# Kernel optimization log

Measured on AMD Instinct MI355X. Metric: run time of the kernel, lower is better.

Reference implementation:

```python
import jax, jax.numpy as jnp
import numpy as np

EPS_BN = 1e-3   # nn.BatchNorm1d(eps=0.001)
LAMDA = 1e-5    # Point_Attentation.lamda


def _bn(x, g, b, m, v):
    # inference-mode BatchNorm1d over last dim
    return (x - m) * (g * jax.lax.rsqrt(v + EPS_BN)) + b


def _forward(features_low, features_high,
             bott_W, bott_b, bott_gamma, bott_beta, bott_mean, bott_var,
             qkv_W, qkv_gamma, qkv_beta, qkv_mean, qkv_var,
             mlp_W, mlp_gamma, mlp_beta, mlp_mean, mlp_var,
             fus_W, fus_b, fus_gamma, fus_beta, fus_mean, fus_var,
             batch_size):
    N, C = features_low.shape
    B = batch_size
    n = N // B  # points per batch segment (equal-length segments)

    # ---- Point_Attentation: per-point channel mean, var over channels / (n-1) ----
    x = features_low
    mean = jnp.mean(x, axis=-1, keepdims=True)
    d = x - mean
    var = jnp.sum(d * d, axis=-1, keepdims=True) / (n - 1)
    e_t = d * d / (4.0 * (var + LAMDA)) + 0.5
    x = x + jax.nn.sigmoid(e_t) * x

    for i in range(3):
        y = jax.nn.relu(_bn(x @ bott_W[2 * i] + bott_b[2 * i],
                            bott_gamma[2 * i], bott_beta[2 * i], bott_mean[2 * i], bott_var[2 * i]))
        y = jax.nn.relu(_bn(y @ bott_W[2 * i + 1] + bott_b[2 * i + 1],
                            bott_gamma[2 * i + 1], bott_beta[2 * i + 1], bott_mean[2 * i + 1], bott_var[2 * i + 1]))
        x = x + y

    # ---- fusion: per-batch QKV attention between low (x) and high features ----
    low = x.reshape(B, n, C)
    high = features_high.reshape(B, n, C)

    q = _bn(jnp.einsum('bnc,cd->bnd', low, qkv_W[0]), qkv_gamma[0], qkv_beta[0], qkv_mean[0], qkv_var[0])
    k = _bn(jnp.einsum('bnc,cd->bnd', high, qkv_W[1]), qkv_gamma[1], qkv_beta[1], qkv_mean[1], qkv_var[1])
    v = _bn(jnp.einsum('bnc,cd->bnd', high, qkv_W[2]), qkv_gamma[2], qkv_beta[2], qkv_mean[2], qkv_var[2])

    scale = 1.0 / jnp.sqrt(jnp.asarray(256.0, dtype=q.dtype))  # normal_dim = 256
    attn = jax.nn.softmax(jnp.einsum('bqc,bkc->bqk', q, k) * scale, axis=-1)
    ao = jnp.einsum('bqk,bkc->bqc', attn, v)

    # mlp: (Linear no-bias -> BN -> Dropout(eval=id) -> ReLU) x2
    h = jax.nn.relu(_bn(jnp.einsum('bnc,cd->bnd', ao, mlp_W[0]), mlp_gamma[0], mlp_beta[0], mlp_mean[0], mlp_var[0]))
    h = jax.nn.relu(_bn(jnp.einsum('bnc,cd->bnd', h, mlp_W[1]), mlp_gamma[1], mlp_beta[1], mlp_mean[1], mlp_var[1]))

    # linear_fusion: Linear(2C->C, bias) -> BN -> ReLU
    cat = jnp.concatenate([low, h], axis=-1)  # [B, n, 2C]
    out = jax.nn.relu(_bn(jnp.einsum('bnc,cd->bnd', cat, fus_W) + fus_b, fus_gamma, fus_beta, fus_mean, fus_var))
    return out.reshape(N, C)


def setup_inputs() -> dict:
    key = jax.random.key(0)
    ks = jax.random.split(key, 16)
    N, C, B = 16384, 256, 4
    s = 0.05
    d = {}
    d['features_low'] = jax.random.normal(ks[0], (N, C), jnp.float32)
    d['features_high'] = jax.random.normal(ks[1], (N, C), jnp.float32)
    d['bott_W'] = jax.random.normal(ks[2], (6, C, C), jnp.float32) * s
    d['bott_b'] = jnp.zeros((6, C), jnp.float32)
    d['bott_gamma'] = jnp.ones((6, C), jnp.float32)
    d['bott_beta'] = jnp.zeros((6, C), jnp.float32)
    d['bott_mean'] = jnp.zeros((6, C), jnp.float32)
    d['bott_var'] = jnp.ones((6, C), jnp.float32)
    d['qkv_W'] = jax.random.normal(ks[3], (3, C, C), jnp.float32) * s
    d['qkv_gamma'] = jnp.ones((3, C), jnp.float32)
    d['qkv_beta'] = jnp.zeros((3, C), jnp.float32)
    d['qkv_mean'] = jnp.zeros((3, C), jnp.float32)
    d['qkv_var'] = jnp.ones((3, C), jnp.float32)
    d['mlp_W'] = jax.random.normal(ks[4], (2, C, C), jnp.float32) * s
    d['mlp_gamma'] = jnp.ones((2, C), jnp.float32)
    d['mlp_beta'] = jnp.zeros((2, C), jnp.float32)
    d['mlp_mean'] = jnp.zeros((2, C), jnp.float32)
    d['mlp_var'] = jnp.ones((2, C), jnp.float32)
    d['fus_W'] = jax.random.normal(ks[5], (2 * C, C), jnp.float32) * s
    d['fus_b'] = jnp.zeros((C,), jnp.float32)
    d['fus_gamma'] = jnp.ones((C,), jnp.float32)
    d['fus_beta'] = jnp.zeros((C,), jnp.float32)
    d['fus_mean'] = jnp.zeros((C,), jnp.float32)
    d['fus_var'] = jnp.ones((C,), jnp.float32)
    d['batch_size'] = B
    return d


def reference(features_low, features_high,
              bott_W, bott_b, bott_gamma, bott_beta, bott_mean, bott_var,
              qkv_W, qkv_gamma, qkv_beta, qkv_mean, qkv_var,
              mlp_W, mlp_gamma, mlp_beta, mlp_mean, mlp_var,
              fus_W, fus_b, fus_gamma, fus_beta, fus_mean, fus_var,
              batch_size):
    return _forward(features_low, features_high,
                    bott_W, bott_b, bott_gamma, bott_beta, bott_mean, bott_var,
                    qkv_W, qkv_gamma, qkv_beta, qkv_mean, qkv_var,
                    mlp_W, mlp_gamma, mlp_beta, mlp_mean, mlp_var,
                    fus_W, fus_b, fus_gamma, fus_beta, fus_mean, fus_var,
                    batch_size)
```

## Files before the change

### kernel.cpp

```cpp
#include <hip/hip_runtime.h>
#include <cstdint>
#include <cstddef>

typedef float v4f __attribute__((ext_vector_type(4)));
typedef float v2f __attribute__((ext_vector_type(2)));
typedef float v16f __attribute__((ext_vector_type(16)));
typedef short v8s __attribute__((ext_vector_type(8)));
typedef unsigned short v4u __attribute__((ext_vector_type(4)));

typedef unsigned short ubf;

#define NPTS 16384
#define CD   256
#define NBAT 4
#define NPB  4096

__device__ __forceinline__ float bf2f(ubf u) {
    union { unsigned u; float f; } c; c.u = ((unsigned)u) << 16; return c.f;
}
__device__ __forceinline__ ubf f2bf(float f) {
    union { float f; unsigned u; } c; c.f = f;
    unsigned u = c.u;
    u += 0x7fffu + ((u >> 16) & 1u);
    return (ubf)(u >> 16);
}

__global__ __launch_bounds__(256) void k_pre(
    const float* __restrict__ low, float* __restrict__ xout,
    const float* __restrict__ bott, const float* __restrict__ qkv,
    const float* __restrict__ mlp, const float* __restrict__ fus,
    ubf* __restrict__ wt) {
    const int bid = blockIdx.x;
    if (bid < 4096) {
        const int lane = threadIdx.x & 63;
        const int row  = bid * 4 + (threadIdx.x >> 6);
        const float* p = low + (size_t)row * CD + lane * 4;
        v4f v = *reinterpret_cast<const v4f*>(p);
        float d[4];
        float s = v[0] + v[1] + v[2] + v[3];
#pragma unroll
        for (int o = 32; o >= 1; o >>= 1) s += __shfl_xor(s, o);
        const float mean = s * (1.0f / 256.0f);
        float ss = 0.f;
#pragma unroll
        for (int i = 0; i < 4; ++i) { d[i] = v[i] - mean; ss += d[i] * d[i]; }
#pragma unroll
        for (int o = 32; o >= 1; o >>= 1) ss += __shfl_xor(ss, o);
        const float var = ss * (1.0f / 4095.0f);
        const float dn  = 1.0f / (4.0f * (var + 1e-5f));
        v4f o;
#pragma unroll
        for (int i = 0; i < 4; ++i) {
            const float e   = d[i] * d[i] * dn + 0.5f;
            const float sig = 1.0f / (1.0f + __expf(-e));
            o[i] = v[i] * (1.0f + sig);
        }
        *reinterpret_cast<v4f*>(xout + (size_t)row * CD + lane * 4) = o;
        return;
    }
    const int bid2 = bid - 4096;
    const int z = bid2 >> 7, r = bid2 & 127;
    const float* src; int K; size_t doff;
    if (z < 6)       { src = bott + (size_t)z * 65536;       K = 256; doff = (size_t)z * 65536; }
    else if (z < 9)  { src = qkv  + (size_t)(z - 6) * 65536; K = 256; doff = (size_t)z * 65536; }
    else if (z < 11) { src = mlp  + (size_t)(z - 9) * 65536; K = 256; doff = (size_t)z * 65536; }
    else             { src = fus;                            K = 512; doff = (size_t)11 * 65536; }
    const int kt = (r >> 3) * 32, nt = (r & 7) * 32;
    if (kt >= K) return;
    __shared__ ubf tile[32][33];
    const int tx = threadIdx.x & 31, ty = threadIdx.x >> 5;
#pragma unroll
    for (int i = 0; i < 4; ++i)
        tile[ty * 4 + i][tx] = f2bf(src[(size_t)(kt + ty * 4 + i) * 256 + nt + tx]);
    __syncthreads();
    ubf* dst = wt + doff;
#pragma unroll
    for (int i = 0; i < 4; ++i)
        dst[(size_t)(nt + ty * 4 + i) * K + kt + tx] = tile[tx][ty * 4 + i];
}

__global__ __launch_bounds__(256) void k_conv1(
    float* __restrict__ xA, const ubf* __restrict__ wT,
    const float* __restrict__ bb, const float* __restrict__ bg,
    const float* __restrict__ bbe, const float* __restrict__ bm_,
    const float* __restrict__ bv) {
    __shared__ __attribute__((aligned(16))) float xls[64 * 256];
    __shared__ __attribute__((aligned(16))) ubf   yls[64 * 256];

    const int lane = threadIdx.x & 63;
    const int w    = threadIdx.x >> 6;
    const int wr = w >> 1, wc = w & 1;
    const int q15 = lane & 15, g = lane >> 4;
    const int bm = blockIdx.x * 64;

    {
        float* xsrcb = xA + (size_t)bm * 256;
#pragma unroll
        for (int it = 0; it < 16; ++it) {
            const int L4 = (it * 256 + w * 64) * 4;
            const int Ll = L4 + lane * 4;
            const int row = Ll >> 8, col = (Ll & 255) ^ ((row & 7) << 3);
            __builtin_amdgcn_global_load_lds(
                (const __attribute__((address_space(1))) unsigned*)(xsrcb + row * 256 + col),
                (__attribute__((address_space(3))) unsigned*)(xls + L4), 16, 0, 0);
        }
    }
    __syncthreads();

    const int r0l = wr * 32 + q15;
#pragma unroll 1
    for (int s = 0; s < 3; ++s) {
        const ubf* W0 = wT + (size_t)(2 * s) * 65536;
        const ubf* W1 = wT + (size_t)(2 * s + 1) * 65536;

        v4f acc[2][8];
#pragma unroll
        for (int i = 0; i < 2; ++i)
#pragma unroll
            for (int j = 0; j < 8; ++j)
#pragma unroll
                for (int r = 0; r < 4; ++r) acc[i][j][r] = 0.f;
        for (int ks = 0; ks < 8; ++ks) {
            const int k0 = ks * 32 + g * 8;
            v8s afr[2], bfr[8];
#pragma unroll
            for (int mi = 0; mi < 2; ++mi) {
                const int row = r0l + mi * 16;
                const float* ap = &xls[row * 256 + (k0 ^ ((row & 7) << 3))];
                v4f a = *reinterpret_cast<const v4f*>(ap);
                v4f b = *reinterpret_cast<const v4f*>(ap + 4);
                v8s t;
#pragma unroll
                for (int j = 0; j < 4; ++j) { t[j] = (short)f2bf(a[j]); t[j + 4] = (short)f2bf(b[j]); }
                afr[mi] = t;
            }
#pragma unroll
            for (int ni = 0; ni < 8; ++ni)
                bfr[ni] = *reinterpret_cast<const v8s*>(W0 + (size_t)(wc * 128 + ni * 16 + q15) * 256 + k0);
#pragma unroll
            for (int mi = 0; mi < 2; ++mi)
#pragma unroll
                for (int ni = 0; ni < 8; ++ni)
                    acc[mi][ni] = __builtin_amdgcn_mfma_f32_16x16x32_bf16(afr[mi], bfr[ni], acc[mi][ni], 0, 0, 0);
        }
#pragma unroll
        for (int ni = 0; ni < 8; ++ni) {
            const int col = wc * 128 + ni * 16 + q15;
            const float sc  = bg[2 * s * 256 + col] * rsqrtf(bv[2 * s * 256 + col] + 1e-3f);
            const float tc  = bbe[2 * s * 256 + col] - bm_[2 * s * 256 + col] * sc;
            const float bia = bb[2 * s * 256 + col];
#pragma unroll
            for (int mi = 0; mi < 2; ++mi)
#pragma unroll
                for (int r = 0; r < 4; ++r) {
                    const int row = wr * 32 + mi * 16 + g * 4 + r;
                    float z = fmaxf((acc[mi][ni][r] + bia) * sc + tc, 0.f);
                    yls[row * 256 + (col ^ ((row & 7) << 3))] = f2bf(z);
                }
        }
        __syncthreads();

#pragma unroll
        for (int i = 0; i < 2; ++i)
#pragma unroll
            for (int j = 0; j < 8; ++j)
#pragma unroll
                for (int r = 0; r < 4; ++r) acc[i][j][r] = 0.f;
        for (int ks = 0; ks < 8; ++ks) {
            const int k0 = ks * 32 + g * 8;
            v8s afr[2], bfr[8];
#pragma unroll
            for (int mi = 0; mi < 2; ++mi) {
                const int row = r0l + mi * 16;
                afr[mi] = *reinterpret_cast<const v8s*>(&yls[row * 256 + (k0 ^ ((row & 7) << 3))]);
            }
#pragma unroll
            for (int ni = 0; ni < 8; ++ni)
                bfr[ni] = *reinterpret_cast<const v8s*>(W1 + (size_t)(wc * 128 + ni * 16 + q15) * 256 + k0);
#pragma unroll
            for (int mi = 0; mi < 2; ++mi)
#pragma unroll
                for (int ni = 0; ni < 8; ++ni)
                    acc[mi][ni] = __builtin_amdgcn_mfma_f32_16x16x32_bf16(afr[mi], bfr[ni], acc[mi][ni], 0, 0, 0);
        }
#pragma unroll
        for (int ni = 0; ni < 8; ++ni) {
            const int col = wc * 128 + ni * 16 + q15;
            const int c1 = (2 * s + 1) * 256 + col;
            const float sc  = bg[c1] * rsqrtf(bv[c1] + 1e-3f);
            const float tc  = bbe[c1] - bm_[c1] * sc;
            const float bia = bb[c1];
#pragma unroll
            for (int mi = 0; mi < 2; ++mi)
#pragma unroll
                for (int r = 0; r < 4; ++r) {
                    const int row = wr * 32 + mi * 16 + g * 4 + r;
                    float z = fmaxf((acc[mi][ni][r] + bia) * sc + tc, 0.f);
                    xls[row * 256 + (col ^ ((row & 7) << 3))] += z;
                }
        }
        __syncthreads();
    }

    {
        float* xdstb = xA + (size_t)bm * 256;
#pragma unroll
        for (int it = 0; it < 16; ++it) {
            const int Ll = (it * 256 + threadIdx.x) * 4;
            const int row = Ll >> 8, cl = Ll & 255;
            const int gcol = cl ^ ((row & 7) << 3);
            *reinterpret_cast<v4f*>(xdstb + row * 256 + gcol) =
                *reinterpret_cast<const v4f*>(xls + Ll);
        }
    }
}

__global__ __launch_bounds__(256) void k_qkv(
    const float* __restrict__ xA, const float* __restrict__ fh,
    const ubf* __restrict__ wTq,
    const float* __restrict__ qg, const float* __restrict__ qbe,
    const float* __restrict__ qm, const float* __restrict__ qv,
    ubf* __restrict__ qB, ubf* __restrict__ kB, ubf* __restrict__ vT) {
    const int m = blockIdx.y >> 1;
    const float* Af = (m == 0) ? xA : fh;
    const ubf* WT = wTq + m * 65536;
    const float* gamma = qg + m * 256;
    const float* beta  = qbe + m * 256;
    const float* bmean = qm + m * 256;
    const float* bvar  = qv + m * 256;

    const int lane = threadIdx.x & 63;
    const int w    = threadIdx.x >> 6;
    const int wr = w >> 1, wc = w & 1;
    const int q15 = lane & 15, g = lane >> 4;
    const int bm = blockIdx.x * 128, bn = (blockIdx.y & 1) * 128;
    const int r0 = bm + wr * 64 + q15;
    const int c0 = bn + wc * 64 + q15;

    v4f acc[4][4];
#pragma unroll
    for (int i = 0; i < 4; ++i)
#pragma unroll
        for (int j = 0; j < 4; ++j)
#pragma unroll
            for (int r = 0; r < 4; ++r) acc[i][j][r] = 0.f;

    for (int ks = 0; ks < 8; ++ks) {
        const int k0 = ks * 32 + g * 8;
        v8s afr[4], bfr[4];
#pragma unroll
        for (int mi = 0; mi < 4; ++mi) {
            const float* ap = Af + (size_t)(r0 + mi * 16) * CD + k0;
            v4f a = *reinterpret_cast<const v4f*>(ap);
            v4f b = *reinterpret_cast<const v4f*>(ap + 4);
            v8s t;
#pragma unroll
            for (int j = 0; j < 4; ++j) { t[j] = (short)f2bf(a[j]); t[j + 4] = (short)f2bf(b[j]); }
            afr[mi] = t;
        }
#pragma unroll
        for (int ni = 0; ni < 4; ++ni)
            bfr[ni] = *reinterpret_cast<const v8s*>(WT + (size_t)(c0 + ni * 16) * 256 + k0);
#pragma unroll
        for (int mi = 0; mi < 4; ++mi)
#pragma unroll
            for (int ni = 0; ni < 4; ++ni)
                acc[mi][ni] = __builtin_amdgcn_mfma_f32_16x16x32_bf16(afr[mi], bfr[ni], acc[mi][ni], 0, 0, 0);
    }

    ubf* outb = (m == 0) ? qB : kB;
#pragma unroll
    for (int ni = 0; ni < 4; ++ni) {
        const int col = c0 + ni * 16;
        const float sc = gamma[col] * rsqrtf(bvar[col] + 1e-3f);
        const float tc = beta[col] - bmean[col] * sc;
#pragma unroll
        for (int mi = 0; mi < 4; ++mi) {
            if (m == 2) {
                const int row0 = bm + wr * 64 + mi * 16 + g * 4;
                v4u pk;
#pragma unroll
                for (int r = 0; r < 4; ++r) pk[r] = f2bf(acc[mi][ni][r] * sc + tc);
                const int bb = row0 >> 12, key = row0 & 4095;
                const int ch = key >> 5, kin = key & 31;
                *reinterpret_cast<v4u*>(vT + (size_t)bb * (CD * NPB)
                                           + (size_t)ch * (CD * 32) + col * 32 + kin) = pk;
            } else {
#pragma unroll
                for (int r = 0; r < 4; ++r) {
                    const int row = bm + wr * 64 + mi * 16 + g * 4 + r;
                    outb[(size_t)row * CD + col] = f2bf(acc[mi][ni][r] * sc + tc);
                }
            }
        }
    }
}

__device__ __forceinline__ void stage_k32(const ubf* __restrict__ kg,
                                          ubf* kd, int wave, int lane) {
#pragma unroll
    for (int it = 0; it < 8; ++it) {
        const int Lb = it * 1024 + wave * 512;
        const int L  = Lb + lane * 8;
        const int key = L >> 8, c8 = (L & 255) ^ ((key & 7) << 3);
        __builtin_amdgcn_global_load_lds(
            (const __attribute__((address_space(1))) unsigned*)(kg + key * CD + c8),
            (__attribute__((address_space(3))) unsigned*)(kd + Lb), 16, 0, 0);
    }
}
__device__ __forceinline__ void stage_v40(const ubf* __restrict__ vchunk,
                                          ubf* vd, int wave, int lane) {
#pragma unroll
    for (int it = 0; it < 10; ++it) {
        const int e0b = wave * 5120 + it * 512;
        const int e0  = e0b + lane * 8;
        const int c   = e0 / 40;
        const int k0  = e0 - c * 40;
        const ubf* src = (k0 < 32) ? (vchunk + c * 32 + k0) : vchunk;
        __builtin_amdgcn_global_load_lds(
            (const __attribute__((address_space(1))) unsigned*)src,
            (__attribute__((address_space(3))) unsigned*)(vd + e0b), 16, 0, 0);
    }
}

__global__ __launch_bounds__(128, 1) void k_attn(const ubf* __restrict__ qb, const ubf* __restrict__ kb,
                                                 const ubf* __restrict__ vt,
                                                 ubf* __restrict__ o0, ubf* __restrict__ o1,
                                                 float* __restrict__ ml) {
    __shared__ __attribute__((aligned(16))) ubf kls[32 * 256];
    __shared__ __attribute__((aligned(16))) ubf vls[256 * 40];
    __shared__ __attribute__((aligned(16))) ubf pls[2 * 32 * 40];

    const int raw = blockIdx.x;
    const int xcd = raw & 7, qt = raw >> 3;
    const int b = xcd >> 1, half = xcd & 1;

    const int wave = threadIdx.x >> 6, lane = threadIdx.x & 63;
    const int q31 = lane & 31, h = lane >> 5;

    const ubf* qrow = qb + ((size_t)(b * NPB + qt * 64 + wave * 32 + q31)) * CD + h * 8;
    v8s qf[16];
#pragma unroll
    for (int ks = 0; ks < 16; ++ks) qf[ks] = *reinterpret_cast<const v8s*>(qrow + ks * 16);

    v16f oacc[8];
#pragma unroll
    for (int t = 0; t < 8; ++t)
#pragma unroll
        for (int r = 0; r < 16; ++r) oacc[t][r] = 0.f;
    float m_run = -3.0e38f, l_run = 0.f;

    const ubf* kgb = kb + ((size_t)(b * NPB) + half * 2048) * CD;
    const ubf* vgb = vt + (size_t)b * (CD * NPB) + (size_t)(half * 64) * (CD * 32);
    ubf* pw = pls + wave * (32 * 40);

    stage_k32(kgb, kls, wave, lane);
    stage_v40(vgb, vls, wave, lane);
    __syncthreads();

    for (int kc = 0; kc < 64; ++kc) {
        v16f sacc;
#pragma unroll
        for (int r = 0; r < 16; ++r) sacc[r] = 0.f;
#pragma unroll
        for (int ks = 0; ks < 16; ++ks) {
            v8s af = *reinterpret_cast<const v8s*>(
                &kls[q31 * 256 + ((ks * 16 + h * 8) ^ ((q31 & 7) << 3))]);
            sacc = __builtin_amdgcn_mfma_f32_32x32x16_bf16(af, qf[ks], sacc, 0, 0, 0);
        }

        __syncthreads();
        if (kc + 1 < 64)
            stage_k32(kgb + (size_t)(kc + 1) * 32 * CD, kls, wave, lane);

        float mloc = -3.0e38f;
#pragma unroll
        for (int r = 0; r < 16; ++r) {
            float x = sacc[r] * 0.0625f;
            sacc[r] = x;
            mloc = fmaxf(mloc, x);
        }
        mloc = fmaxf(mloc, __shfl_xor(mloc, 32));
        if (!__all(mloc <= m_run + 8.0f)) {
            const float mnew  = fmaxf(m_run, mloc);
            const float alpha = __expf(m_run - mnew);
            l_run *= alpha;
#pragma unroll
            for (int t = 0; t < 8; ++t)
#pragma unroll
                for (int r = 0; r < 16; ++r) oacc[t][r] *= alpha;
            m_run = mnew;
        }
        float lloc = 0.f;
#pragma unroll
        for (int r = 0; r < 16; ++r) {
            float p = __expf(sacc[r] - m_run);
            sacc[r] = p;
            lloc += p;
        }
        lloc += __shfl_xor(lloc, 32);
        l_run += lloc;

#pragma unroll
        for (int G = 0; G < 4; ++G) {
            unsigned u0, u1, u2, u3;
            { union { float f; unsigned u; } c; c.f = sacc[4 * G + 0]; u0 = c.u; }
            { union { float f; unsigned u; } c; c.f = sacc[4 * G + 1]; u1 = c.u; }
            { union { float f; unsigned u; } c; c.f = sacc[4 * G + 2]; u2 = c.u; }
            { union { float f; unsigned u; } c; c.f = sacc[4 * G + 3]; u3 = c.u; }
            unsigned p01 = (u0 >> 16) | (u1 & 0xFFFF0000u);
            unsigned p23 = (u2 >> 16) | (u3 & 0xFFFF0000u);
            const int e = q31 * 40 + 8 * G + 4 * h;
            *reinterpret_cast<unsigned*>(&pw[e])     = p01;
            *reinterpret_cast<unsigned*>(&pw[e + 2]) = p23;
        }
        v8s pb0 = *reinterpret_cast<const v8s*>(&pw[q31 * 40 + 0  + 8 * h]);
        v8s pb1 = *reinterpret_cast<const v8s*>(&pw[q31 * 40 + 16 + 8 * h]);
#pragma unroll
        for (int t = 0; t < 8; ++t) {
            const int crow = (t * 32 + q31) * 40;
            v8s av0 = *reinterpret_cast<const v8s*>(&vls[crow + 0  + 8 * h]);
            oacc[t] = __builtin_amdgcn_mfma_f32_32x32x16_bf16(av0, pb0, oacc[t], 0, 0, 0);
            v8s av1 = *reinterpret_cast<const v8s*>(&vls[crow + 16 + 8 * h]);
            oacc[t] = __builtin_amdgcn_mfma_f32_32x32x16_bf16(av1, pb1, oacc[t], 0, 0, 0);
        }

        __syncthreads();
        if (kc + 1 < 64)
            stage_v40(vgb + (size_t)(kc + 1) * (CD * 32), vls, wave, lane);
    }

    const int grow = b * NPB + qt * 64 + wave * 32 + q31;
    ubf* aor = (half ? o1 : o0) + (size_t)grow * CD;
#pragma unroll
    for (int t = 0; t < 8; ++t)
#pragma unroll
        for (int G = 0; G < 4; ++G) {
            v4u pk;
#pragma unroll
            for (int r = 0; r < 4; ++r) pk[r] = f2bf(oacc[t][4 * G + r]);
            *reinterpret_cast<v4u*>(aor + t * 32 + 8 * G + 4 * h) = pk;
        }
    if (h == 0) {
        v2f d; d[0] = m_run; d[1] = l_run;
        *reinterpret_cast<v2f*>(ml + (size_t)(half * NPTS + grow) * 2) = d;
    }
}

__global__ __launch_bounds__(256) void k_tail(
    const ubf* __restrict__ o0, const ubf* __restrict__ o1, const float* __restrict__ ml,
    const float* __restrict__ xA, const ubf* __restrict__ wT,
    const float* __restrict__ mg, const float* __restrict__ mbe,
    const float* __restrict__ mm, const float* __restrict__ mv,
    const float* __restrict__ fb, const float* __restrict__ fg,
    const float* __restrict__ fbe, const float* __restrict__ fm,
    const float* __restrict__ fv, float* __restrict__ out) {
    __shared__ __attribute__((aligned(16))) ubf yls[64 * 256];

    const int lane = threadIdx.x & 63;
    const int w    = threadIdx.x >> 6;
    const int wr = w >> 1, wc = w & 1;
    const int q15 = lane & 15, g = lane >> 4;
    const int bm = blockIdx.x * 64;
    const int r0l = wr * 32 + q15;

    const ubf* W9  = wT + (size_t)9 * 65536;
    const ubf* W10 = wT + (size_t)10 * 65536;
    const ubf* W11 = wT + (size_t)11 * 65536;

    v4f acc[2][8];

    float a0[2], a1[2];
#pragma unroll
    for (int mi = 0; mi < 2; ++mi) {
        const int row = bm + r0l + mi * 16;
        const float m0 = ml[2 * row],          l0 = ml[2 * row + 1];
        const float m1 = ml[2 * (NPTS + row)], l1 = ml[2 * (NPTS + row) + 1];
        const float mx = fmaxf(m0, m1);
        const float w0 = __expf(m0 - mx), w1 = __expf(m1 - mx);
        const float inv = 1.0f / (w0 * l0 + w1 * l1);
        a0[mi] = w0 * inv; a1[mi] = w1 * inv;
    }
#pragma unroll
    for (int i = 0; i < 2; ++i)
#pragma unroll
        for (int j = 0; j < 8; ++j)
#pragma unroll
            for (int r = 0; r < 4; ++r) acc[i][j][r] = 0.f;
    for (int ks = 0; ks < 8; ++ks) {
        const int k0 = ks * 32 + g * 8;
        v8s afr[2], bfr[8];
#pragma unroll
        for (int mi = 0; mi < 2; ++mi) {
            const int row = bm + r0l + mi * 16;
            v8s u0 = *reinterpret_cast<const v8s*>(o0 + (size_t)row * CD + k0);
            v8s u1 = *reinterpret_cast<const v8s*>(o1 + (size_t)row * CD + k0);
            v8s t;
#pragma unroll
            for (int j = 0; j < 8; ++j)
                t[j] = (short)f2bf(a0[mi] * bf2f((ubf)u0[j]) + a1[mi] * bf2f((ubf)u1[j]));
            afr[mi] = t;
        }
#pragma unroll
        for (int ni = 0; ni < 8; ++ni)
            bfr[ni] = *reinterpret_cast<const v8s*>(W9 + (size_t)(wc * 128 + ni * 16 + q15) * 256 + k0);
#pragma unroll
        for (int mi = 0; mi < 2; ++mi)
#pragma unroll
            for (int ni = 0; ni < 8; ++ni)
                acc[mi][ni] = __builtin_amdgcn_mfma_f32_16x16x32_bf16(afr[mi], bfr[ni], acc[mi][ni], 0, 0, 0);
    }
#pragma unroll
    for (int ni = 0; ni < 8; ++ni) {
        const int col = wc * 128 + ni * 16 + q15;
        const float sc = mg[col] * rsqrtf(mv[col] + 1e-3f);
        const float tc = mbe[col] - mm[col] * sc;
#pragma unroll
        for (int mi = 0; mi < 2; ++mi)
#pragma unroll
            for (int r = 0; r < 4; ++r) {
                const int row = wr * 32 + mi * 16 + g * 4 + r;
                float z = fmaxf(acc[mi][ni][r] * sc + tc, 0.f);
                yls[row * 256 + (col ^ ((row & 7) << 3))] = f2bf(z);
            }
    }
    __syncthreads();

#pragma unroll
    for (int i = 0; i < 2; ++i)
#pragma unroll
        for (int j = 0; j < 8; ++j)
#pragma unroll
            for (int r = 0; r < 4; ++r) acc[i][j][r] = 0.f;
    for (int ks = 0; ks < 8; ++ks) {
        const int k0 = ks * 32 + g * 8;
        v8s afr[2], bfr[8];
#pragma unroll
        for (int mi = 0; mi < 2; ++mi) {
            const int row = r0l + mi * 16;
            afr[mi] = *reinterpret_cast<const v8s*>(&yls[row * 256 + (k0 ^ ((row & 7) << 3))]);
        }
#pragma unroll
        for (int ni = 0; ni < 8; ++ni)
            bfr[ni] = *reinterpret_cast<const v8s*>(W10 + (size_t)(wc * 128 + ni * 16 + q15) * 256 + k0);
#pragma unroll
        for (int mi = 0; mi < 2; ++mi)
#pragma unroll
            for (int ni = 0; ni < 8; ++ni)
                acc[mi][ni] = __builtin_amdgcn_mfma_f32_16x16x32_bf16(afr[mi], bfr[ni], acc[mi][ni], 0, 0, 0);
    }
    __syncthreads();
#pragma unroll
    for (int ni = 0; ni < 8; ++ni) {
        const int col = wc * 128 + ni * 16 + q15;
        const float sc = mg[256 + col] * rsqrtf(mv[256 + col] + 1e-3f);
        const float tc = mbe[256 + col] - mm[256 + col] * sc;
#pragma unroll
        for (int mi = 0; mi < 2; ++mi)
#pragma unroll
            for (int r = 0; r < 4; ++r) {
                const int row = wr * 32 + mi * 16 + g * 4 + r;
                float z = fmaxf(acc[mi][ni][r] * sc + tc, 0.f);
                yls[row * 256 + (col ^ ((row & 7) << 3))] = f2bf(z);
            }
    }
    __syncthreads();

#pragma unroll
    for (int i = 0; i < 2; ++i)
#pragma unroll
        for (int j = 0; j < 8; ++j)
#pragma unroll
            for (int r = 0; r < 4; ++r) acc[i][j][r] = 0.f;
    for (int ks = 0; ks < 16; ++ks) {
        const int k0 = ks * 32 + g * 8;
        v8s afr[2], bfr[8];
#pragma unroll
        for (int mi = 0; mi < 2; ++mi) {
            if (k0 < 256) {
                const float* ap = xA + (size_t)(bm + r0l + mi * 16) * CD + k0;
                v4f a = *reinterpret_cast<const v4f*>(ap);
                v4f b = *reinterpret_cast<const v4f*>(ap + 4);
                v8s t;
#pragma unroll
                for (int j = 0; j < 4; ++j) { t[j] = (short)f2bf(a[j]); t[j + 4] = (short)f2bf(b[j]); }
                afr[mi] = t;
            } else {
                const int row = r0l + mi * 16, kk = k0 - 256;
                afr[mi] = *reinterpret_cast<const v8s*>(&yls[row * 256 + (kk ^ ((row & 7) << 3))]);
            }
        }
#pragma unroll
        for (int ni = 0; ni < 8; ++ni)
            bfr[ni] = *reinterpret_cast<const v8s*>(W11 + (size_t)(wc * 128 + ni * 16 + q15) * 512 + k0);
#pragma unroll
        for (int mi = 0; mi < 2; ++mi)
#pragma unroll
            for (int ni = 0; ni < 8; ++ni)
                acc[mi][ni] = __builtin_amdgcn_mfma_f32_16x16x32_bf16(afr[mi], bfr[ni], acc[mi][ni], 0, 0, 0);
    }
#pragma unroll
    for (int ni = 0; ni < 8; ++ni) {
        const int col = wc * 128 + ni * 16 + q15;
        const float sc = fg[col] * rsqrtf(fv[col] + 1e-3f);
        const float tc = fbe[col] - fm[col] * sc;
        const float bia = fb[col];
#pragma unroll
        for (int mi = 0; mi < 2; ++mi)
#pragma unroll
            for (int r = 0; r < 4; ++r) {
                const int row = bm + wr * 32 + mi * 16 + g * 4 + r;
                float z = fmaxf((acc[mi][ni][r] + bia) * sc + tc, 0.f);
                out[(size_t)row * CD + col] = z;
            }
    }
}

extern "C" void kernel_launch(void* const* d_in, const int* in_sizes, int n_in,
                              void* d_out, int out_size, void* d_ws, size_t ws_size,
                              hipStream_t stream) {
    const float* f_low   = (const float*)d_in[0];
    const float* f_high  = (const float*)d_in[1];
    const float* bott_W  = (const float*)d_in[2];
    const float* bott_b  = (const float*)d_in[3];
    const float* bott_g  = (const float*)d_in[4];
    const float* bott_be = (const float*)d_in[5];
    const float* bott_m  = (const float*)d_in[6];
    const float* bott_v  = (const float*)d_in[7];
    const float* qkv_W   = (const float*)d_in[8];
    const float* qkv_g   = (const float*)d_in[9];
    const float* qkv_be  = (const float*)d_in[10];
    const float* qkv_m   = (const float*)d_in[11];
    const float* qkv_v   = (const float*)d_in[12];
    const float* mlp_W   = (const float*)d_in[13];
    const float* mlp_g   = (const float*)d_in[14];
    const float* mlp_be  = (const float*)d_in[15];
    const float* mlp_m   = (const float*)d_in[16];
    const float* mlp_v   = (const float*)d_in[17];
    const float* fus_W   = (const float*)d_in[18];
    const float* fus_b   = (const float*)d_in[19];
    const float* fus_g   = (const float*)d_in[20];
    const float* fus_be  = (const float*)d_in[21];
    const float* fus_m   = (const float*)d_in[22];
    const float* fus_v   = (const float*)d_in[23];
    (void)in_sizes; (void)n_in; (void)out_size; (void)ws_size;

    char* ws = (char*)d_ws;
    const size_t MB = 1024 * 1024;
    float* xA = (float*)(ws);
    ubf*   o0 = (ubf*)  (ws + 17 * MB);
    ubf*   qB = (ubf*)  (ws + 26 * MB);
    ubf*   kB = (ubf*)  (ws + 35 * MB);
    ubf*   vT = (ubf*)  (ws + 44 * MB);
    ubf*   wT = (ubf*)  (ws + 53 * MB);
    ubf*   o1 = (ubf*)  (ws + 56 * MB);
    float* ml = (float*)(ws + 65 * MB);

    k_pre<<<dim3(4096 + 1536), dim3(256), 0, stream>>>(f_low, xA,
                                                       bott_W, qkv_W, mlp_W, fus_W, wT);

    k_conv1<<<dim3(256), dim3(256), 0, stream>>>(xA, wT,
                                                 bott_b, bott_g, bott_be, bott_m, bott_v);

    k_qkv<<<dim3(128, 6), dim3(256), 0, stream>>>(xA, f_high, wT + (size_t)6 * 65536,
                                                  qkv_g, qkv_be, qkv_m, qkv_v, qB, kB, vT);

    k_attn<<<dim3(512), dim3(128), 0, stream>>>(qB, kB, vT, o0, o1, ml);

    k_tail<<<dim3(256), dim3(256), 0, stream>>>(o0, o1, ml, xA, wT,
                                                mlp_g, mlp_be, mlp_m, mlp_v,
                                                fus_b, fus_g, fus_be, fus_m, fus_v,
                                                (float*)d_out);
}
```

Measured before the change: 287.1 us.

## Fuse Q projection into conv1 and double-buffer K/V tiles in attention

The Q projection is computed inside k_conv1 straight from the residual tile already held in LDS, so the fp32 activations are not reread from global memory. K and V get their own launch that reads only the high features. The attention kernel now double-buffers the K and V LDS tiles and prefetches the next chunk at the top of each iteration, which removes one barrier per iteration. LDS use in k_attn roughly doubles and conv1 does more work per block, which may lower occupancy or lengthen the conv1 critical path.

Result: no change. 292.2 us (+1.8%).

```diff
diff --git a/kernel.cpp b/kernel.cpp
--- a/kernel.cpp
+++ b/kernel.cpp
@@ -83,7 +83,10 @@
     float* __restrict__ xA, const ubf* __restrict__ wT,
     const float* __restrict__ bb, const float* __restrict__ bg,
     const float* __restrict__ bbe, const float* __restrict__ bm_,
-    const float* __restrict__ bv) {
+    const float* __restrict__ bv,
+    const float* __restrict__ qg, const float* __restrict__ qbe,
+    const float* __restrict__ qm, const float* __restrict__ qv,
+    ubf* __restrict__ qB) {
     __shared__ __attribute__((aligned(16))) float xls[64 * 256];
     __shared__ __attribute__((aligned(16))) ubf   yls[64 * 256];
 
@@ -213,16 +216,61 @@
                 *reinterpret_cast<const v4f*>(xls + Ll);
         }
     }
-}
-
-__global__ __launch_bounds__(256) void k_qkv(
-    const float* __restrict__ xA, const float* __restrict__ fh,
-    const ubf* __restrict__ wTq,
+
+    {
+        const ubf* WQ = wT + (size_t)6 * 65536;
+        v4f acc[2][8];
+#pragma unroll
+        for (int i = 0; i < 2; ++i)
+#pragma unroll
+            for (int j = 0; j < 8; ++j)
+#pragma unroll
+                for (int r = 0; r < 4; ++r) acc[i][j][r] = 0.f;
+        for (int ks = 0; ks < 8; ++ks) {
+            const int k0 = ks * 32 + g * 8;
+            v8s afr[2], bfr[8];
+#pragma unroll
+            for (int mi = 0; mi < 2; ++mi) {
+                const int row = r0l + mi * 16;
+                const float* ap = &xls[row * 256 + (k0 ^ ((row & 7) << 3))];
+                v4f a = *reinterpret_cast<const v4f*>(ap);
+                v4f b = *reinterpret_cast<const v4f*>(ap + 4);
+                v8s t;
+#pragma unroll
+                for (int j = 0; j < 4; ++j) { t[j] = (short)f2bf(a[j]); t[j + 4] = (short)f2bf(b[j]); }
+                afr[mi] = t;
+            }
+#pragma unroll
+            for (int ni = 0; ni < 8; ++ni)
+                bfr[ni] = *reinterpret_cast<const v8s*>(WQ + (size_t)(wc * 128 + ni * 16 + q15) * 256 + k0);
+#pragma unroll
+            for (int mi = 0; mi < 2; ++mi)
+#pragma unroll
+                for (int ni = 0; ni < 8; ++ni)
+                    acc[mi][ni] = __builtin_amdgcn_mfma_f32_16x16x32_bf16(afr[mi], bfr[ni], acc[mi][ni], 0, 0, 0);
+        }
+#pragma unroll
+        for (int ni = 0; ni < 8; ++ni) {
+            const int col = wc * 128 + ni * 16 + q15;
+            const float sc = qg[col] * rsqrtf(qv[col] + 1e-3f);
+            const float tc = qbe[col] - qm[col] * sc;
+#pragma unroll
+            for (int mi = 0; mi < 2; ++mi)
+#pragma unroll
+                for (int r = 0; r < 4; ++r) {
+                    const int row = bm + wr * 32 + mi * 16 + g * 4 + r;
+                    qB[(size_t)row * CD + col] = f2bf(acc[mi][ni][r] * sc + tc);
+                }
+        }
+    }
+}
+
+__global__ __launch_bounds__(256) void k_kv(
+    const float* __restrict__ fh, const ubf* __restrict__ wTq,
     const float* __restrict__ qg, const float* __restrict__ qbe,
     const float* __restrict__ qm, const float* __restrict__ qv,
-    ubf* __restrict__ qB, ubf* __restrict__ kB, ubf* __restrict__ vT) {
-    const int m = blockIdx.y >> 1;
-    const float* Af = (m == 0) ? xA : fh;
+    ubf* __restrict__ kB, ubf* __restrict__ vT) {
+    const int m = 1 + (blockIdx.y >> 1);
     const ubf* WT = wTq + m * 65536;
     const float* gamma = qg + m * 256;
     const float* beta  = qbe + m * 256;
@@ -250,7 +298,7 @@
         v8s afr[4], bfr[4];
 #pragma unroll
         for (int mi = 0; mi < 4; ++mi) {
-            const float* ap = Af + (size_t)(r0 + mi * 16) * CD + k0;
+            const float* ap = fh + (size_t)(r0 + mi * 16) * CD + k0;
             v4f a = *reinterpret_cast<const v4f*>(ap);
             v4f b = *reinterpret_cast<const v4f*>(ap + 4);
             v8s t;
@@ -268,7 +316,6 @@
                 acc[mi][ni] = __builtin_amdgcn_mfma_f32_16x16x32_bf16(afr[mi], bfr[ni], acc[mi][ni], 0, 0, 0);
     }
 
-    ubf* outb = (m == 0) ? qB : kB;
 #pragma unroll
     for (int ni = 0; ni < 4; ++ni) {
         const int col = c0 + ni * 16;
@@ -289,7 +336,7 @@
 #pragma unroll
                 for (int r = 0; r < 4; ++r) {
                     const int row = bm + wr * 64 + mi * 16 + g * 4 + r;
-                    outb[(size_t)row * CD + col] = f2bf(acc[mi][ni][r] * sc + tc);
+                    kB[(size_t)row * CD + col] = f2bf(acc[mi][ni][r] * sc + tc);
                 }
             }
         }
@@ -327,8 +374,8 @@
                                                  const ubf* __restrict__ vt,
                                                  ubf* __restrict__ o0, ubf* __restrict__ o1,
                                                  float* __restrict__ ml) {
-    __shared__ __attribute__((aligned(16))) ubf kls[32 * 256];
-    __shared__ __attribute__((aligned(16))) ubf vls[256 * 40];
+    __shared__ __attribute__((aligned(16))) ubf kbuf[2][32 * 256];
+    __shared__ __attribute__((aligned(16))) ubf vbuf[2][256 * 40];
     __shared__ __attribute__((aligned(16))) ubf pls[2 * 32 * 40];
 
     const int raw = blockIdx.x;
@@ -354,11 +401,20 @@
     const ubf* vgb = vt + (size_t)b * (CD * NPB) + (size_t)(half * 64) * (CD * 32);
     ubf* pw = pls + wave * (32 * 40);
 
-    stage_k32(kgb, kls, wave, lane);
-    stage_v40(vgb, vls, wave, lane);
+    stage_k32(kgb, kbuf[0], wave, lane);
+    stage_v40(vgb, vbuf[0], wave, lane);
     __syncthreads();
 
     for (int kc = 0; kc < 64; ++kc) {
+        const int cur = kc & 1;
+        const ubf* kls = kbuf[cur];
+        const ubf* vls = vbuf[cur];
+
+        if (kc + 1 < 64) {
+            stage_k32(kgb + (size_t)(kc + 1) * 32 * CD, kbuf[cur ^ 1], wave, lane);
+            stage_v40(vgb + (size_t)(kc + 1) * (CD * 32), vbuf[cur ^ 1], wave, lane);
+        }
+
         v16f sacc;
 #pragma unroll
         for (int r = 0; r < 16; ++r) sacc[r] = 0.f;
@@ -368,10 +424,6 @@
                 &kls[q31 * 256 + ((ks * 16 + h * 8) ^ ((q31 & 7) << 3))]);
             sacc = __builtin_amdgcn_mfma_f32_32x32x16_bf16(af, qf[ks], sacc, 0, 0, 0);
         }
-
-        __syncthreads();
-        if (kc + 1 < 64)
-            stage_k32(kgb + (size_t)(kc + 1) * 32 * CD, kls, wave, lane);
 
         float mloc = -3.0e38f;
 #pragma unroll
@@ -426,8 +478,6 @@
         }
 
         __syncthreads();
-        if (kc + 1 < 64)
-            stage_v40(vgb + (size_t)(kc + 1) * (CD * 32), vls, wave, lane);
     }
 
     const int grow = b * NPB + qt * 64 + wave * 32 + q31;
@@ -659,11 +709,12 @@
     k_pre<<<dim3(4096 + 1536), dim3(256), 0, stream>>>(f_low, xA,
                                                        bott_W, qkv_W, mlp_W, fus_W, wT);
 
+    k_kv<<<dim3(128, 4), dim3(256), 0, stream>>>(f_high, wT + (size_t)6 * 65536,
+                                                 qkv_g, qkv_be, qkv_m, qkv_v, kB, vT);
+
     k_conv1<<<dim3(256), dim3(256), 0, stream>>>(xA, wT,
-                                                 bott_b, bott_g, bott_be, bott_m, bott_v);
-
-    k_qkv<<<dim3(128, 6), dim3(256), 0, stream>>>(xA, f_high, wT + (size_t)6 * 65536,
-                                                  qkv_g, qkv_be, qkv_m, qkv_v, qB, kB, vT);
+                                                 bott_b, bott_g, bott_be, bott_m, bott_v,
+                                                 qkv_g, qkv_be, qkv_m, qkv_v, qB);
 
     k_attn<<<dim3(512), dim3(128), 0, stream>>>(qB, kB, vT, o0, o1, ml);
 
```
